# Kernel optimization log

Measured on AMD Instinct MI355X. Metric: run time of the kernel, lower is better.

## Reference

```python
import jax, jax.numpy as jnp
import numpy as np

N_HEAD = 16
ROPE_BASE = 10000.0

def _rotate_half(x):
    # matches torch: stack((-x[...,1::2], x[...,::2]), -1).flatten(-2)
    x1 = x[..., ::2]
    x2 = x[..., 1::2]
    return jnp.stack((-x2, x1), axis=-1).reshape(x.shape)

def setup_inputs() -> dict:
    key = jax.random.key(0)
    ks = jax.random.split(key, 5)
    B, T, C = 4, 2048, 1024
    x = jax.random.normal(ks[0], (B, T, C), dtype=jnp.float32)
    Wq = jax.random.normal(ks[1], (C, C), dtype=jnp.float32) * 0.02
    Wk = jax.random.normal(ks[2], (C, C), dtype=jnp.float32) * 0.02
    Wv = jax.random.normal(ks[3], (C, C), dtype=jnp.float32) * 0.02
    Wp = jax.random.normal(ks[4], (C, C), dtype=jnp.float32) * 0.02
    return {"x": x, "Wq": Wq, "Wk": Wk, "Wv": Wv, "Wp": Wp, "start_pos": 0}

def reference(x, Wq, Wk, Wv, Wp, start_pos):
    B, T, C = x.shape
    H = N_HEAD
    D = C // H
    # torch Linear: out = x @ W^T
    q = jnp.einsum('btc,dc->btd', x, Wq).reshape(B, T, H, D).transpose(0, 2, 1, 3)
    k = jnp.einsum('btc,dc->btd', x, Wk).reshape(B, T, H, D).transpose(0, 2, 1, 3)
    v = jnp.einsum('btc,dc->btd', x, Wv).reshape(B, T, H, D).transpose(0, 2, 1, 3)
    # RoPE cache (cat[freqs, freqs] with interleaved rotate_half, as in source)
    inv_freq = 1.0 / (ROPE_BASE ** (jnp.arange(0, D, 2, dtype=jnp.float32) / D))
    t = jnp.arange(T, dtype=jnp.float32) + jnp.float32(start_pos)
    freqs = t[:, None] * inv_freq[None, :]          # [T, D/2]
    emb = jnp.concatenate([freqs, freqs], axis=-1)  # [T, D]
    cos = jnp.cos(emb)[None, None]                  # [1,1,T,D]
    sin = jnp.sin(emb)[None, None]
    q = q * cos + _rotate_half(q) * sin
    k = k * cos + _rotate_half(k) * sin
    att = jnp.einsum('bhqd,bhkd->bhqk', q, k) / jnp.sqrt(jnp.float32(D))
    mask = jnp.triu(jnp.ones((T, T), dtype=bool), k=1)
    att = jnp.where(mask, -jnp.inf, att)
    att = jax.nn.softmax(att, axis=-1)
    y = jnp.einsum('bhqk,bhkd->bhqd', att, v)
    y = y.transpose(0, 2, 1, 3).reshape(B, T, C)
    return jnp.einsum('btc,dc->btd', y, Wp)
```

## Files before the change

kernel.cpp:

```cpp
#include <hip/hip_runtime.h>
#include <hip/hip_bf16.h>
#include <stdint.h>

#define B_  4
#define T_  2048
#define C_  1024
#define H_  16
#define D_  64
#define BT  (B_*T_)
#define KDIM 1024

typedef __attribute__((ext_vector_type(8))) short bf16x8;
typedef __attribute__((ext_vector_type(4))) float f32x4;

__device__ __forceinline__ unsigned short f2bf(float f) {
  union { float f; unsigned u; } v; v.f = f;
  unsigned r = v.u + 0x7FFFu + ((v.u >> 16) & 1u);
  return (unsigned short)(r >> 16);
}

__device__ __forceinline__ float exp2_fast(float x) {
  float r;
  asm("v_exp_f32 %0, %1" : "=v"(r) : "v"(x));
  return r;
}

__device__ __forceinline__ void gld_lds16(const void* g, void* l) {
  __builtin_amdgcn_global_load_lds(
      (__attribute__((address_space(1))) unsigned int*)(uintptr_t)g,
      (__attribute__((address_space(3))) unsigned int*)(unsigned)(uintptr_t)l,
      16, 0, 0);
}

__global__ __launch_bounds__(256) void k_convert(
    const float* __restrict__ x,  const float* __restrict__ wq,
    const float* __restrict__ wk, const float* __restrict__ wv,
    const float* __restrict__ wp,
    unsigned short* __restrict__ xb, unsigned short* __restrict__ wcat,
    unsigned short* __restrict__ wpb)
{
  const int NX = BT*C_/4;
  const int NW = C_*C_/4;
  const int TOT = NX + 4*NW;
  for (int i = blockIdx.x*blockDim.x + threadIdx.x; i < TOT; i += gridDim.x*blockDim.x) {
    const float4* src; unsigned short* dst; int idx;
    if (i < NX)                { src = (const float4*)x;  dst = xb;            idx = i; }
    else {
      int j = i - NX;
      if (j < NW)              { src = (const float4*)wq; dst = wcat;          idx = j; }
      else if (j < 2*NW)       { src = (const float4*)wk; dst = wcat + C_*C_;  idx = j - NW; }
      else if (j < 3*NW)       { src = (const float4*)wv; dst = wcat + 2*C_*C_;idx = j - 2*NW; }
      else                     { src = (const float4*)wp; dst = wpb;           idx = j - 3*NW; }
    }
    float4 v = src[idx];
    ushort4 o; o.x = f2bf(v.x); o.y = f2bf(v.y); o.z = f2bf(v.z); o.w = f2bf(v.w);
    *(ushort4*)(dst + (size_t)idx*4) = o;
  }
}

__global__ __launch_bounds__(256) void k_rope_tab(
    const int* __restrict__ start_pos, float* __restrict__ cosT, float* __restrict__ sinT)
{
  int i = blockIdx.x*blockDim.x + threadIdx.x;
  if (i >= T_*D_) return;
  int t = i >> 6, j = i & 63;
  float inv = exp2f(-(float)(j & 31) * (13.287712379549449f / 32.0f));
  float ang = (float)(t + start_pos[0]) * inv;
  cosT[i] = cosf(ang);
  sinT[i] = sinf(ang);
}

__global__ __launch_bounds__(512, 2) void k_gemm256(
    const unsigned short* __restrict__ A, const unsigned short* __restrict__ Bw,
    unsigned short* __restrict__ qb, unsigned short* __restrict__ kb,
    unsigned short* __restrict__ vt,
    const float* __restrict__ cosT, const float* __restrict__ sinT)
{
  __shared__ __attribute__((aligned(16))) char smem[131072];
  const int tid = threadIdx.x, l = tid & 63, w = tid >> 6;
  const int g = l >> 4, c = l & 15;
  const int m0 = blockIdx.x * 256, n0 = blockIdx.y * 256;
  const int wr = w >> 2, wc = w & 3;
  const char* gA = (const char*)A;
  const char* gB = (const char*)Bw;

  int dstU[2]; size_t aoff[2], boff[2];
#pragma unroll
  for (int j = 0; j < 2; ++j) {
    int P = j*8192 + tid*16;
    int p = P >> 7;
    int inner = (P & 127) ^ ((p & 7) << 4);
    int row = (p << 1) | (inner >> 6);
    int kc = (inner & 63) >> 1;
    dstU[j] = P;
    aoff[j] = ((size_t)(m0 + row) * KDIM + kc) * 2;
    boff[j] = ((size_t)(n0 + row) * KDIM + kc) * 2;
  }

  const int swzo = ((((c & 1) << 6) | (g << 4)) ^ (((c >> 1) & 7) << 4));
  const int aB = (wr*64 + (c >> 1)) * 128 + swzo;
  const int bB = 32768 + (wc*32 + (c >> 1)) * 128 + swzo;

  f32x4 acc[8][4];
#pragma unroll
  for (int i = 0; i < 8; ++i)
#pragma unroll
    for (int j = 0; j < 4; ++j) acc[i][j] = (f32x4){0.f,0.f,0.f,0.f};

#pragma unroll
  for (int j = 0; j < 2; ++j) gld_lds16(gA + aoff[j],      smem +     0 + dstU[j]);
#pragma unroll
  for (int j = 0; j < 2; ++j) gld_lds16(gB + boff[j],      smem + 32768 + dstU[j]);
#pragma unroll
  for (int j = 0; j < 2; ++j) gld_lds16(gA + aoff[j] + 64, smem + 16384 + dstU[j]);
#pragma unroll
  for (int j = 0; j < 2; ++j) gld_lds16(gB + boff[j] + 64, smem + 49152 + dstU[j]);
  asm volatile("s_waitcnt vmcnt(4)" ::: "memory");
  __builtin_amdgcn_s_barrier();

#define MFMA16(MB)                                                               \
    __builtin_amdgcn_s_setprio(1);                                               \
    _Pragma("unroll")                                                            \
    for (int i2 = 0; i2 < 4; ++i2)                                               \
      _Pragma("unroll")                                                          \
      for (int ni = 0; ni < 4; ++ni)                                             \
        acc[(MB)+i2][ni] = __builtin_amdgcn_mfma_f32_16x16x32_bf16(              \
            af[i2], bk[ni], acc[(MB)+i2][ni], 0, 0, 0);                          \
    __builtin_amdgcn_s_setprio(0);

#define PRE_MFMA                                                                 \
    __builtin_amdgcn_s_barrier();                                                \
    asm volatile("s_waitcnt lgkmcnt(0)" ::: "memory");                           \
    __builtin_amdgcn_sched_barrier(0);

  bf16x8 af[4], bk[4];

#pragma unroll 2
  for (int t = 0; t < 15; ++t) {
    const int par = (t & 1) << 16;
    const int nxt = par ^ 65536;
    const size_t ko = (size_t)(t + 1) * 128;

#pragma unroll
    for (int i2 = 0; i2 < 4; ++i2) af[i2] = *(const bf16x8*)(smem + par + aB + i2*1024);
#pragma unroll
    for (int ni = 0; ni < 4; ++ni) bk[ni] = *(const bf16x8*)(smem + par + bB + ni*1024);
#pragma unroll
    for (int j = 0; j < 2; ++j) gld_lds16(gA + aoff[j] + ko, smem + nxt + dstU[j]);
    PRE_MFMA
    MFMA16(0)
    __builtin_amdgcn_s_barrier();

#pragma unroll
    for (int i2 = 0; i2 < 4; ++i2) af[i2] = *(const bf16x8*)(smem + par + aB + (4+i2)*1024);
#pragma unroll
    for (int j = 0; j < 2; ++j) gld_lds16(gB + boff[j] + ko, smem + nxt + 32768 + dstU[j]);
    PRE_MFMA
    MFMA16(4)
    asm volatile("s_waitcnt vmcnt(4)" ::: "memory");
    __builtin_amdgcn_s_barrier();

#pragma unroll
    for (int i2 = 0; i2 < 4; ++i2) af[i2] = *(const bf16x8*)(smem + par + 16384 + aB + i2*1024);
#pragma unroll
    for (int ni = 0; ni < 4; ++ni) bk[ni] = *(const bf16x8*)(smem + par + 16384 + bB + ni*1024);
#pragma unroll
    for (int j = 0; j < 2; ++j) gld_lds16(gA + aoff[j] + ko + 64, smem + nxt + 16384 + dstU[j]);
    PRE_MFMA
    MFMA16(0)
    __builtin_amdgcn_s_barrier();

#pragma unroll
    for (int i2 = 0; i2 < 4; ++i2) af[i2] = *(const bf16x8*)(smem + par + 16384 + aB + (4+i2)*1024);
#pragma unroll
    for (int j = 0; j < 2; ++j) gld_lds16(gB + boff[j] + ko + 64, smem + nxt + 49152 + dstU[j]);
    PRE_MFMA
    MFMA16(4)
    asm volatile("s_waitcnt vmcnt(4)" ::: "memory");
    __builtin_amdgcn_s_barrier();
  }

  {
    const int par = 65536;
#pragma unroll
    for (int i2 = 0; i2 < 4; ++i2) af[i2] = *(const bf16x8*)(smem + par + aB + i2*1024);
#pragma unroll
    for (int ni = 0; ni < 4; ++ni) bk[ni] = *(const bf16x8*)(smem + par + bB + ni*1024);
    PRE_MFMA
    MFMA16(0)
    __builtin_amdgcn_s_barrier();
#pragma unroll
    for (int i2 = 0; i2 < 4; ++i2) af[i2] = *(const bf16x8*)(smem + par + aB + (4+i2)*1024);
    PRE_MFMA
    MFMA16(4)
    asm volatile("s_waitcnt vmcnt(0)" ::: "memory");
    __builtin_amdgcn_s_barrier();
#pragma unroll
    for (int i2 = 0; i2 < 4; ++i2) af[i2] = *(const bf16x8*)(smem + par + 16384 + aB + i2*1024);
#pragma unroll
    for (int ni = 0; ni < 4; ++ni) bk[ni] = *(const bf16x8*)(smem + par + 16384 + bB + ni*1024);
    PRE_MFMA
    MFMA16(0)
    __builtin_amdgcn_s_barrier();
#pragma unroll
    for (int i2 = 0; i2 < 4; ++i2) af[i2] = *(const bf16x8*)(smem + par + 16384 + aB + (4+i2)*1024);
    PRE_MFMA
    MFMA16(4)
  }
#undef MFMA16
#undef PRE_MFMA

#pragma unroll
  for (int mi = 0; mi < 8; ++mi) {
#pragma unroll
    for (int ni = 0; ni < 4; ++ni) {
      const int mrow0 = m0 + wr*128 + mi*16 + g*4;
      const int ncol  = n0 + wc*64 + ni*16 + c;
      const int which = ncol >> 10;
      const int d = ncol & 1023, h = d >> 6, dd = d & 63;
      const int b = mrow0 >> 11, t0 = mrow0 & 2047;
      if (which == 2) {
        ushort4 o;
        o.x = f2bf(acc[mi][ni][0]); o.y = f2bf(acc[mi][ni][1]);
        o.z = f2bf(acc[mi][ni][2]); o.w = f2bf(acc[mi][ni][3]);
        *(ushort4*)(vt + ((size_t)((b*H_ + h)*D_ + dd))*T_ + t0) = o;
      } else {
#pragma unroll
        for (int r = 0; r < 4; ++r) {
          float val = acc[mi][ni][r];
          float partner = __shfl_xor(val, 1);
          float rot = (dd & 1) ? partner : -partner;
          float cv = cosT[(t0 + r)*64 + dd], sv = sinT[(t0 + r)*64 + dd];
          float o = val*cv + rot*sv;
          size_t oidx = (((size_t)(b*H_ + h))*T_ + (t0 + r))*D_ + dd;
          if (which == 0) qb[oidx] = f2bf(o * 0.180336879f);
          else            kb[oidx] = f2bf(o);
        }
      }
    }
  }
}

template<int EPI>
__global__ __launch_bounds__(256) void k_gemm(
    const unsigned short* __restrict__ A, const unsigned short* __restrict__ Bw,
    unsigned short* __restrict__ qb, unsigned short* __restrict__ kb,
    unsigned short* __restrict__ vt,
    const float* __restrict__ cosT, const float* __restrict__ sinT,
    float* __restrict__ outF)
{
  __shared__ __attribute__((aligned(16))) char smem[32768];
  const int tid = threadIdx.x, l = tid & 63, w = tid >> 6;
  const int g = l >> 4, c = l & 15;
  const int m0 = blockIdx.x * 128, n0 = blockIdx.y * 128;
  const int wr = w >> 1, wc = w & 1;

  const char* srcA[4]; const char* srcB[4]; int dstP[4];
#pragma unroll
  for (int j = 0; j < 4; ++j) {
    int P = w*4096 + j*1024 + l*16;
    int row = P >> 7;
    int Lb = P ^ ((row & 7) << 4);
    int col = (Lb & 127) >> 1;
    dstP[j] = P;
    srcA[j] = (const char*)A  + ((size_t)(m0 + row) * KDIM + col) * 2;
    srcB[j] = (const char*)Bw + ((size_t)(n0 + row) * KDIM + col) * 2;
  }

  f32x4 acc[4][4];
#pragma unroll
  for (int i = 0; i < 4; ++i)
#pragma unroll
    for (int j = 0; j < 4; ++j) acc[i][j] = (f32x4){0.f,0.f,0.f,0.f};

  for (int kt = 0; kt < KDIM; kt += 64) {
#pragma unroll
    for (int j = 0; j < 4; ++j) {
      gld_lds16(srcA[j] + kt*2, smem + dstP[j]);
      gld_lds16(srcB[j] + kt*2, smem + 16384 + dstP[j]);
    }
    __syncthreads();
#pragma unroll
    for (int kk = 0; kk < 2; ++kk) {
      bf16x8 af[4], bw4[4];
#pragma unroll
      for (int mi = 0; mi < 4; ++mi) {
        int row = wr*64 + mi*16 + c;
        int Lb = row*128 + (kk*32 + g*8)*2;
        af[mi] = *(const bf16x8*)(smem + (Lb ^ ((row & 7) << 4)));
      }
#pragma unroll
      for (int ni = 0; ni < 4; ++ni) {
        int row = wc*64 + ni*16 + c;
        int Lb = row*128 + (kk*32 + g*8)*2;
        bw4[ni] = *(const bf16x8*)(smem + 16384 + (Lb ^ ((row & 7) << 4)));
      }
#pragma unroll
      for (int mi = 0; mi < 4; ++mi)
#pragma unroll
        for (int ni = 0; ni < 4; ++ni)
          acc[mi][ni] = __builtin_amdgcn_mfma_f32_16x16x32_bf16(af[mi], bw4[ni], acc[mi][ni], 0, 0, 0);
    }
    __syncthreads();
  }

#pragma unroll
  for (int mi = 0; mi < 4; ++mi) {
#pragma unroll
    for (int ni = 0; ni < 4; ++ni) {
      const int mrow0 = m0 + wr*64 + mi*16 + g*4;
      const int ncol  = n0 + wc*64 + ni*16 + c;
      if (EPI == 1) {
#pragma unroll
        for (int r = 0; r < 4; ++r)
          outF[(size_t)(mrow0 + r) * 1024 + ncol] = acc[mi][ni][r];
      } else {
        const int which = ncol >> 10;
        const int d = ncol & 1023, h = d >> 6, dd = d & 63;
        const int b = mrow0 >> 11, t0 = mrow0 & 2047;
        if (which == 2) {
          ushort4 o;
          o.x = f2bf(acc[mi][ni][0]); o.y = f2bf(acc[mi][ni][1]);
          o.z = f2bf(acc[mi][ni][2]); o.w = f2bf(acc[mi][ni][3]);
          *(ushort4*)(vt + ((size_t)((b*H_ + h)*D_ + dd))*T_ + t0) = o;
        } else {
#pragma unroll
          for (int r = 0; r < 4; ++r) {
            float val = acc[mi][ni][r];
            float partner = __shfl_xor(val, 1);
            float rot = (dd & 1) ? partner : -partner;
            float cv = cosT[(t0 + r)*64 + dd], sv = sinT[(t0 + r)*64 + dd];
            float o = val*cv + rot*sv;
            size_t oidx = (((size_t)(b*H_ + h))*T_ + (t0 + r))*D_ + dd;
            if (which == 0) qb[oidx] = f2bf(o * 0.180336879f);
            else            kb[oidx] = f2bf(o);
          }
        }
      }
    }
  }
}

__global__ __launch_bounds__(256) void k_attn(
    const unsigned short* __restrict__ qb, const unsigned short* __restrict__ kb,
    const unsigned short* __restrict__ vt, unsigned short* __restrict__ yb)
{
  __shared__ __attribute__((aligned(16))) char smem[65536];
  const int tid = threadIdx.x, l = tid & 63, w = tid >> 6;
  const int g = l >> 4, c = l & 15;
  const int bh = blockIdx.x;
  const int pidx = blockIdx.y;
  const size_t bhO = (size_t)bh * T_ * D_;
  const int pbase = 49152 + w*4096;
  const int b = bh >> 4, h = bh & 15;

  bf16x8 vones;
#pragma unroll
  for (int i = 0; i < 8; ++i) vones[i] = (short)0x3F80;

  const char* srcK[2]; const char* srcV[2]; int dstP2[2];
#pragma unroll
  for (int j = 0; j < 2; ++j) {
    int P = w*2048 + j*1024 + l*16;
    int row = P >> 7;
    int Lb = P ^ ((row & 7) << 4);
    int col = (Lb & 127) >> 1;
    dstP2[j] = P;
    srcK[j] = (const char*)(kb + bhO) + ((size_t)row*D_ + col)*2;
    srcV[j] = (const char*)(vt + bhO) + ((size_t)row*T_ + col)*2;
  }

  for (int half = 0; half < 2; ++half) {
    const int qt = half ? pidx : (15 - pidx);
    const int q0 = qt * 128;
    const int q0w = q0 + w*32;

    bf16x8 aq[2][2];
#pragma unroll
    for (int mi = 0; mi < 2; ++mi)
#pragma unroll
      for (int kc = 0; kc < 2; ++kc) {
        int row = q0w + mi*16 + c;
        aq[mi][kc] = *(const bf16x8*)(qb + bhO + (size_t)row*D_ + kc*32 + g*8);
      }

    f32x4 po[4][2];
    f32x4 ls[2];
    float mrun[2];
#pragma unroll
    for (int nd = 0; nd < 4; ++nd)
#pragma unroll
      for (int mi = 0; mi < 2; ++mi) po[nd][mi] = (f32x4){0.f,0.f,0.f,0.f};
    ls[0] = (f32x4){0.f,0.f,0.f,0.f}; ls[1] = (f32x4){0.f,0.f,0.f,0.f};
    mrun[0] = mrun[1] = -1e30f;

    const int nkt = (q0 + 128) >> 6;

#pragma unroll
    for (int j = 0; j < 2; ++j) {
      gld_lds16(srcK[j], smem + dstP2[j]);
      gld_lds16(srcV[j], smem + 8192 + dstP2[j]);
    }
#pragma unroll
    for (int j = 0; j < 2; ++j) {
      gld_lds16(srcK[j] + (size_t)64*128, smem + 16384 + dstP2[j]);
      gld_lds16(srcV[j] + (size_t)64*2,   smem + 16384 + 8192 + dstP2[j]);
    }
    asm volatile("s_waitcnt vmcnt(4)" ::: "memory");
    __builtin_amdgcn_s_barrier();
    __builtin_amdgcn_sched_barrier(0);

    int rd = 0;
    for (int it = 0; it < nkt; ++it) {
      const int kv0 = it * 64;
      const int cur = rd * 16384;

      if (it + 2 < nkt) {
        int wi = rd + 2; if (wi >= 3) wi -= 3;
        const int wb = wi * 16384;
        const size_t ko = (size_t)(kv0 + 128) * 128;
        const size_t vo = (size_t)(kv0 + 128) * 2;
#pragma unroll
        for (int j = 0; j < 2; ++j) {
          gld_lds16(srcK[j] + ko, smem + wb + dstP2[j]);
          gld_lds16(srcV[j] + vo, smem + wb + 8192 + dstP2[j]);
        }
      }

      if (kv0 < q0w + 32) {
        f32x4 st[4][2];
#pragma unroll
        for (int ni = 0; ni < 4; ++ni)
#pragma unroll
          for (int mi = 0; mi < 2; ++mi) st[ni][mi] = (f32x4){0.f,0.f,0.f,0.f};
        __builtin_amdgcn_s_setprio(1);
#pragma unroll
        for (int kk = 0; kk < 2; ++kk) {
          bf16x8 bk[4];
#pragma unroll
          for (int ni = 0; ni < 4; ++ni) {
            int kn = ni*16 + c;
            int Lb = kn*128 + (kk*32 + g*8)*2;
            bk[ni] = *(const bf16x8*)(smem + cur + (Lb ^ ((kn & 7) << 4)));
          }
#pragma unroll
          for (int ni = 0; ni < 4; ++ni)
#pragma unroll
            for (int mi = 0; mi < 2; ++mi)
              st[ni][mi] = __builtin_amdgcn_mfma_f32_16x16x32_bf16(bk[ni], aq[mi][kk], st[ni][mi], 0, 0, 0);
        }
        __builtin_amdgcn_s_setprio(0);

        if (kv0 + 64 > q0w) {
#pragma unroll
          for (int ni = 0; ni < 4; ++ni)
#pragma unroll
            for (int r = 0; r < 4; ++r) {
              int kvv = kv0 + ni*16 + g*4 + r;
#pragma unroll
              for (int mi = 0; mi < 2; ++mi) {
                int qq = q0w + mi*16 + c;
                if (kvv > qq) st[ni][mi][r] = -1e30f;
              }
            }
        }

#pragma unroll
        for (int mi = 0; mi < 2; ++mi) {
          float mn[4];
#pragma unroll
          for (int ni = 0; ni < 4; ++ni)
            mn[ni] = fmaxf(fmaxf(st[ni][mi][0], st[ni][mi][1]),
                           fmaxf(st[ni][mi][2], st[ni][mi][3]));
          float mt = fmaxf(fmaxf(mn[0], mn[1]), fmaxf(mn[2], mn[3]));
          mt = fmaxf(mt, __shfl_xor(mt, 16));
          mt = fmaxf(mt, __shfl_xor(mt, 32));
          float m_use = mrun[mi];
          if (__any(mt > m_use + 8.f)) {
            float mnew = fmaxf(m_use, mt);
            float alpha = exp2_fast(m_use - mnew);
            mrun[mi] = mnew;
            m_use = mnew;
#pragma unroll
            for (int r = 0; r < 4; ++r) ls[mi][r] *= alpha;
#pragma unroll
            for (int nd = 0; nd < 4; ++nd)
#pragma unroll
              for (int r = 0; r < 4; ++r) po[nd][mi][r] *= alpha;
          }
#pragma unroll
          for (int ni = 0; ni < 4; ++ni)
#pragma unroll
            for (int r = 0; r < 4; ++r)
              st[ni][mi][r] = exp2_fast(st[ni][mi][r] - m_use);
        }

#pragma unroll
        for (int mi = 0; mi < 2; ++mi) {
          const int row = mi*16 + c;
          const int sw = (row & 7) << 4;
          const int rb = pbase + row*128;
#pragma unroll
          for (int ni = 0; ni < 4; ++ni) {
            unsigned u0, u1;
            asm("v_cvt_pk_bf16_f32 %0, %1, %2" : "=v"(u0) : "v"(st[ni][mi][0]), "v"(st[ni][mi][1]));
            asm("v_cvt_pk_bf16_f32 %0, %1, %2" : "=v"(u1) : "v"(st[ni][mi][2]), "v"(st[ni][mi][3]));
            int Lb = (ni*16 + g*4) * 2;
            uint2 uu; uu.x = u0; uu.y = u1;
            *(uint2*)(smem + rb + (Lb ^ sw)) = uu;
          }
        }

        __builtin_amdgcn_s_setprio(1);
#pragma unroll
        for (int kk = 0; kk < 2; ++kk) {
          bf16x8 pb[2];
#pragma unroll
          for (int mi = 0; mi < 2; ++mi) {
            int pr = mi*16 + c;
            int Lb = pr*128 + (kk*32 + g*8)*2;
            pb[mi] = *(const bf16x8*)(smem + pbase + (Lb ^ ((pr & 7) << 4)));
          }
#pragma unroll
          for (int mi = 0; mi < 2; ++mi)
            ls[mi] = __builtin_amdgcn_mfma_f32_16x16x32_bf16(vones, pb[mi], ls[mi], 0, 0, 0);
          bf16x8 bv[4];
#pragma unroll
          for (int nd = 0; nd < 4; ++nd) {
            int vr = nd*16 + c;
            int Lb = vr*128 + (kk*32 + g*8)*2;
            bv[nd] = *(const bf16x8*)(smem + cur + 8192 + (Lb ^ ((vr & 7) << 4)));
          }
#pragma unroll
          for (int nd = 0; nd < 4; ++nd)
#pragma unroll
            for (int mi = 0; mi < 2; ++mi)
              po[nd][mi] = __builtin_amdgcn_mfma_f32_16x16x32_bf16(bv[nd], pb[mi], po[nd][mi], 0, 0, 0);
        }
        __builtin_amdgcn_s_setprio(0);
      }

      if (it + 1 < nkt) {
        if (it + 2 < nkt) { asm volatile("s_waitcnt vmcnt(4)" ::: "memory"); }
        else              { asm volatile("s_waitcnt vmcnt(0)" ::: "memory"); }
      }
      __builtin_amdgcn_s_barrier();
      __builtin_amdgcn_sched_barrier(0);
      rd = (rd == 2) ? 0 : rd + 1;
    }

#pragma unroll
    for (int mi = 0; mi < 2; ++mi) {
      float inv = 1.f / ls[mi][0];
      int t = q0w + mi*16 + c;
#pragma unroll
      for (int nd = 0; nd < 4; ++nd) {
        ushort4 o;
        o.x = f2bf(po[nd][mi][0] * inv);
        o.y = f2bf(po[nd][mi][1] * inv);
        o.z = f2bf(po[nd][mi][2] * inv);
        o.w = f2bf(po[nd][mi][3] * inv);
        *(ushort4*)(yb + ((size_t)b*T_ + t)*C_ + h*64 + nd*16 + g*4) = o;
      }
    }
  }
}

extern "C" void kernel_launch(void* const* d_in, const int* in_sizes, int n_in,
                              void* d_out, int out_size, void* d_ws, size_t ws_size,
                              hipStream_t stream)
{
  const float* x  = (const float*)d_in[0];
  const float* Wq = (const float*)d_in[1];
  const float* Wk = (const float*)d_in[2];
  const float* Wv = (const float*)d_in[3];
  const float* Wp = (const float*)d_in[4];
  const int*   sp = (const int*)d_in[5];
  float* out = (float*)d_out;

  char* ws = (char*)d_ws;
  unsigned short* xb   = (unsigned short*)(ws);
  unsigned short* wcat = (unsigned short*)(ws + 16777216);
  unsigned short* wpb  = (unsigned short*)(ws + 23068672);
  unsigned short* qb   = (unsigned short*)(ws + 25165824);
  unsigned short* kb   = (unsigned short*)(ws + 41943040);
  unsigned short* vt   = (unsigned short*)(ws + 58720256);
  unsigned short* yb   = (unsigned short*)(ws + 75497472);
  float* cosT = (float*)(ws + 92274688);
  float* sinT = (float*)(ws + 92798976);

  k_convert<<<dim3(2048), dim3(256), 0, stream>>>(x, Wq, Wk, Wv, Wp, xb, wcat, wpb);
  k_rope_tab<<<dim3(512), dim3(256), 0, stream>>>(sp, cosT, sinT);
  k_gemm256<<<dim3(32, 12), dim3(512), 0, stream>>>(xb, wcat, qb, kb, vt, cosT, sinT);
  k_attn<<<dim3(64, 8), dim3(256), 0, stream>>>(qb, kb, vt, yb);
  k_gemm<1><<<dim3(64, 8), dim3(256), 0, stream>>>(yb, wpb, nullptr, nullptr, nullptr, nullptr, nullptr, out);
}
```

Baseline: 186.3 us.

## Split attention query tile across eight waves with sixteen rows each

The attention kernel now launches 512 threads per block, so eight waves each own 16 query rows instead of four waves owning 32. Per-wave register state (accumulators, scores, Q fragments) is halved and the K/V staging load per thread drops to one 16-byte copy per buffer, with the wait counts adjusted to match. The aim is more waves in flight to hide latency and better causal skipping at finer granularity. In exchange each wave reuses every K/V fragment read from shared memory for only one query block, which doubles LDS read traffic per unit of MFMA work.

```diff
diff --git a/kernel.cpp b/kernel.cpp
--- a/kernel.cpp
+++ b/kernel.cpp
@@ -341,7 +341,7 @@
   }
 }
 
-__global__ __launch_bounds__(256) void k_attn(
+__global__ __launch_bounds__(512) void k_attn(
     const unsigned short* __restrict__ qb, const unsigned short* __restrict__ kb,
     const unsigned short* __restrict__ vt, unsigned short* __restrict__ yb)
 {
@@ -351,62 +351,48 @@
   const int bh = blockIdx.x;
   const int pidx = blockIdx.y;
   const size_t bhO = (size_t)bh * T_ * D_;
-  const int pbase = 49152 + w*4096;
+  const int pbase = 49152 + w*2048;
   const int b = bh >> 4, h = bh & 15;
 
   bf16x8 vones;
 #pragma unroll
   for (int i = 0; i < 8; ++i) vones[i] = (short)0x3F80;
 
-  const char* srcK[2]; const char* srcV[2]; int dstP2[2];
-#pragma unroll
-  for (int j = 0; j < 2; ++j) {
-    int P = w*2048 + j*1024 + l*16;
+  const char* srcK; const char* srcV; int dstP2;
+  {
+    int P = w*1024 + l*16;
     int row = P >> 7;
     int Lb = P ^ ((row & 7) << 4);
     int col = (Lb & 127) >> 1;
-    dstP2[j] = P;
-    srcK[j] = (const char*)(kb + bhO) + ((size_t)row*D_ + col)*2;
-    srcV[j] = (const char*)(vt + bhO) + ((size_t)row*T_ + col)*2;
+    dstP2 = P;
+    srcK = (const char*)(kb + bhO) + ((size_t)row*D_ + col)*2;
+    srcV = (const char*)(vt + bhO) + ((size_t)row*T_ + col)*2;
   }
 
   for (int half = 0; half < 2; ++half) {
     const int qt = half ? pidx : (15 - pidx);
     const int q0 = qt * 128;
-    const int q0w = q0 + w*32;
-
-    bf16x8 aq[2][2];
-#pragma unroll
-    for (int mi = 0; mi < 2; ++mi)
-#pragma unroll
-      for (int kc = 0; kc < 2; ++kc) {
-        int row = q0w + mi*16 + c;
-        aq[mi][kc] = *(const bf16x8*)(qb + bhO + (size_t)row*D_ + kc*32 + g*8);
-      }
-
-    f32x4 po[4][2];
-    f32x4 ls[2];
-    float mrun[2];
-#pragma unroll
-    for (int nd = 0; nd < 4; ++nd)
-#pragma unroll
-      for (int mi = 0; mi < 2; ++mi) po[nd][mi] = (f32x4){0.f,0.f,0.f,0.f};
-    ls[0] = (f32x4){0.f,0.f,0.f,0.f}; ls[1] = (f32x4){0.f,0.f,0.f,0.f};
-    mrun[0] = mrun[1] = -1e30f;
+    const int q0w = q0 + w*16;
+
+    bf16x8 aq[2];
+#pragma unroll
+    for (int kc = 0; kc < 2; ++kc)
+      aq[kc] = *(const bf16x8*)(qb + bhO + (size_t)(q0w + c)*D_ + kc*32 + g*8);
+
+    f32x4 po[4];
+    f32x4 ls;
+    float mrun = -1e30f;
+#pragma unroll
+    for (int nd = 0; nd < 4; ++nd) po[nd] = (f32x4){0.f,0.f,0.f,0.f};
+    ls = (f32x4){0.f,0.f,0.f,0.f};
 
     const int nkt = (q0 + 128) >> 6;
 
-#pragma unroll
-    for (int j = 0; j < 2; ++j) {
-      gld_lds16(srcK[j], smem + dstP2[j]);
-      gld_lds16(srcV[j], smem + 8192 + dstP2[j]);
-    }
-#pragma unroll
-    for (int j = 0; j < 2; ++j) {
-      gld_lds16(srcK[j] + (size_t)64*128, smem + 16384 + dstP2[j]);
-      gld_lds16(srcV[j] + (size_t)64*2,   smem + 16384 + 8192 + dstP2[j]);
-    }
-    asm volatile("s_waitcnt vmcnt(4)" ::: "memory");
+    gld_lds16(srcK, smem + dstP2);
+    gld_lds16(srcV, smem + 8192 + dstP2);
+    gld_lds16(srcK + (size_t)64*128, smem + 16384 + dstP2);
+    gld_lds16(srcV + (size_t)64*2,   smem + 16384 + 8192 + dstP2);
+    asm volatile("s_waitcnt vmcnt(2)" ::: "memory");
     __builtin_amdgcn_s_barrier();
     __builtin_amdgcn_sched_barrier(0);
 
@@ -418,21 +404,14 @@
       if (it + 2 < nkt) {
         int wi = rd + 2; if (wi >= 3) wi -= 3;
         const int wb = wi * 16384;
-        const size_t ko = (size_t)(kv0 + 128) * 128;
-        const size_t vo = (size_t)(kv0 + 128) * 2;
-#pragma unroll
-        for (int j = 0; j < 2; ++j) {
-          gld_lds16(srcK[j] + ko, smem + wb + dstP2[j]);
-          gld_lds16(srcV[j] + vo, smem + wb + 8192 + dstP2[j]);
-        }
-      }
-
-      if (kv0 < q0w + 32) {
-        f32x4 st[4][2];
-#pragma unroll
-        for (int ni = 0; ni < 4; ++ni)
-#pragma unroll
-          for (int mi = 0; mi < 2; ++mi) st[ni][mi] = (f32x4){0.f,0.f,0.f,0.f};
+        gld_lds16(srcK + (size_t)(kv0 + 128) * 128, smem + wb + dstP2);
+        gld_lds16(srcV + (size_t)(kv0 + 128) * 2,   smem + wb + 8192 + dstP2);
+      }
+
+      if (kv0 < q0w + 16) {
+        f32x4 st[4];
+#pragma unroll
+        for (int ni = 0; ni < 4; ++ni) st[ni] = (f32x4){0.f,0.f,0.f,0.f};
         __builtin_amdgcn_s_setprio(1);
 #pragma unroll
         for (int kk = 0; kk < 2; ++kk) {
@@ -445,66 +424,58 @@
           }
 #pragma unroll
           for (int ni = 0; ni < 4; ++ni)
-#pragma unroll
-            for (int mi = 0; mi < 2; ++mi)
-              st[ni][mi] = __builtin_amdgcn_mfma_f32_16x16x32_bf16(bk[ni], aq[mi][kk], st[ni][mi], 0, 0, 0);
+            st[ni] = __builtin_amdgcn_mfma_f32_16x16x32_bf16(bk[ni], aq[kk], st[ni], 0, 0, 0);
         }
         __builtin_amdgcn_s_setprio(0);
 
         if (kv0 + 64 > q0w) {
+          const int qq = q0w + c;
 #pragma unroll
           for (int ni = 0; ni < 4; ++ni)
 #pragma unroll
             for (int r = 0; r < 4; ++r) {
               int kvv = kv0 + ni*16 + g*4 + r;
-#pragma unroll
-              for (int mi = 0; mi < 2; ++mi) {
-                int qq = q0w + mi*16 + c;
-                if (kvv > qq) st[ni][mi][r] = -1e30f;
-              }
+              if (kvv > qq) st[ni][r] = -1e30f;
             }
         }
 
-#pragma unroll
-        for (int mi = 0; mi < 2; ++mi) {
+        {
           float mn[4];
 #pragma unroll
           for (int ni = 0; ni < 4; ++ni)
-            mn[ni] = fmaxf(fmaxf(st[ni][mi][0], st[ni][mi][1]),
-                           fmaxf(st[ni][mi][2], st[ni][mi][3]));
+            mn[ni] = fmaxf(fmaxf(st[ni][0], st[ni][1]), fmaxf(st[ni][2], st[ni][3]));
           float mt = fmaxf(fmaxf(mn[0], mn[1]), fmaxf(mn[2], mn[3]));
           mt = fmaxf(mt, __shfl_xor(mt, 16));
           mt = fmaxf(mt, __shfl_xor(mt, 32));
-          float m_use = mrun[mi];
+          float m_use = mrun;
           if (__any(mt > m_use + 8.f)) {
             float mnew = fmaxf(m_use, mt);
             float alpha = exp2_fast(m_use - mnew);
-            mrun[mi] = mnew;
+            mrun = mnew;
             m_use = mnew;
 #pragma unroll
-            for (int r = 0; r < 4; ++r) ls[mi][r] *= alpha;
+            for (int r = 0; r < 4; ++r) ls[r] *= alpha;
 #pragma unroll
             for (int nd = 0; nd < 4; ++nd)
 #pragma unroll
-              for (int r = 0; r < 4; ++r) po[nd][mi][r] *= alpha;
+              for (int r = 0; r < 4; ++r) po[nd][r] *= alpha;
           }
 #pragma unroll
           for (int ni = 0; ni < 4; ++ni)
 #pragma unroll
             for (int r = 0; r < 4; ++r)
-              st[ni][mi][r] = exp2_fast(st[ni][mi][r] - m_use);
-        }
-
-#pragma unroll
-        for (int mi = 0; mi < 2; ++mi) {
-          const int row = mi*16 + c;
+              st[ni][r] = exp2_fast(st[ni][r] - m_use);
+        }
+
+        {
+          const int row = c;
           const int sw = (row & 7) << 4;
           const int rb = pbase + row*128;
 #pragma unroll
           for (int ni = 0; ni < 4; ++ni) {
             unsigned u0, u1;
-            asm("v_cvt_pk_bf16_f32 %0, %1, %2" : "=v"(u0) : "v"(st[ni][mi][0]), "v"(st[ni][mi][1]));
-            asm("v_cvt_pk_bf16_f32 %0, %1, %2" : "=v"(u1) : "v"(st[ni][mi][2]), "v"(st[ni][mi][3]));
+            asm("v_cvt_pk_bf16_f32 %0, %1, %2" : "=v"(u0) : "v"(st[ni][0]), "v"(st[ni][1]));
+            asm("v_cvt_pk_bf16_f32 %0, %1, %2" : "=v"(u1) : "v"(st[ni][2]), "v"(st[ni][3]));
             int Lb = (ni*16 + g*4) * 2;
             uint2 uu; uu.x = u0; uu.y = u1;
             *(uint2*)(smem + rb + (Lb ^ sw)) = uu;
@@ -514,16 +485,13 @@
         __builtin_amdgcn_s_setprio(1);
 #pragma unroll
         for (int kk = 0; kk < 2; ++kk) {
-          bf16x8 pb[2];
-#pragma unroll
-          for (int mi = 0; mi < 2; ++mi) {
-            int pr = mi*16 + c;
+          bf16x8 pb;
+          {
+            int pr = c;
             int Lb = pr*128 + (kk*32 + g*8)*2;
-            pb[mi] = *(const bf16x8*)(smem + pbase + (Lb ^ ((pr & 7) << 4)));
+            pb = *(const bf16x8*)(smem + pbase + (Lb ^ ((pr & 7) << 4)));
           }
-#pragma unroll
-          for (int mi = 0; mi < 2; ++mi)
-            ls[mi] = __builtin_amdgcn_mfma_f32_16x16x32_bf16(vones, pb[mi], ls[mi], 0, 0, 0);
+          ls = __builtin_amdgcn_mfma_f32_16x16x32_bf16(vones, pb, ls, 0, 0, 0);
           bf16x8 bv[4];
 #pragma unroll
           for (int nd = 0; nd < 4; ++nd) {
@@ -533,15 +501,13 @@
           }
 #pragma unroll
           for (int nd = 0; nd < 4; ++nd)
-#pragma unroll
-            for (int mi = 0; mi < 2; ++mi)
-              po[nd][mi] = __builtin_amdgcn_mfma_f32_16x16x32_bf16(bv[nd], pb[mi], po[nd][mi], 0, 0, 0);
+            po[nd] = __builtin_amdgcn_mfma_f32_16x16x32_bf16(bv[nd], pb, po[nd], 0, 0, 0);
         }
         __builtin_amdgcn_s_setprio(0);
       }
 
       if (it + 1 < nkt) {
-        if (it + 2 < nkt) { asm volatile("s_waitcnt vmcnt(4)" ::: "memory"); }
+        if (it + 2 < nkt) { asm volatile("s_waitcnt vmcnt(2)" ::: "memory"); }
         else              { asm volatile("s_waitcnt vmcnt(0)" ::: "memory"); }
       }
       __builtin_amdgcn_s_barrier();
@@ -549,17 +515,16 @@
       rd = (rd == 2) ? 0 : rd + 1;
     }
 
-#pragma unroll
-    for (int mi = 0; mi < 2; ++mi) {
-      float inv = 1.f / ls[mi][0];
-      int t = q0w + mi*16 + c;
+    {
+      float inv = 1.f / ls[0];
+      int t = q0w + c;
 #pragma unroll
       for (int nd = 0; nd < 4; ++nd) {
         ushort4 o;
-        o.x = f2bf(po[nd][mi][0] * inv);
-        o.y = f2bf(po[nd][mi][1] * inv);
-        o.z = f2bf(po[nd][mi][2] * inv);
-        o.w = f2bf(po[nd][mi][3] * inv);
+        o.x = f2bf(po[nd][0] * inv);
+        o.y = f2bf(po[nd][1] * inv);
+        o.z = f2bf(po[nd][2] * inv);
+        o.w = f2bf(po[nd][3] * inv);
         *(ushort4*)(yb + ((size_t)b*T_ + t)*C_ + h*64 + nd*16 + g*4) = o;
       }
     }
@@ -592,6 +557,6 @@
   k_convert<<<dim3(2048), dim3(256), 0, stream>>>(x, Wq, Wk, Wv, Wp, xb, wcat, wpb);
   k_rope_tab<<<dim3(512), dim3(256), 0, stream>>>(sp, cosT, sinT);
   k_gemm256<<<dim3(32, 12), dim3(512), 0, stream>>>(xb, wcat, qb, kb, vt, cosT, sinT);
-  k_attn<<<dim3(64, 8), dim3(256), 0, stream>>>(qb, kb, vt, yb);
+  k_attn<<<dim3(64, 8), dim3(512), 0, stream>>>(qb, kb, vt, yb);
   k_gemm<1><<<dim3(64, 8), dim3(256), 0, stream>>>(yb, wpb, nullptr, nullptr, nullptr, nullptr, nullptr, out);
 }
```

Result: faster. 173.4 us (-6.9%).
